# Optimization experiments

Measured on AMD Instinct MI355X. Metric: run time of the kernel, lower is better.

Reference implementation:

```python
import jax, jax.numpy as jnp
import numpy as np

B, S = 8192, 2048
EPS = 1e-8
DISCOUNT_FACTOR = 0.99
AVERAGE_LAMBDA = 0.9


def setup_inputs() -> dict:
    key = jax.random.key(0)
    k1, k2 = jax.random.split(key)
    values = jax.random.normal(k1, (B, S + 1, 1), dtype=jnp.float32)
    rewards = jax.random.normal(k2, (B, S, 1), dtype=jnp.float32)
    dones = jnp.zeros((B, S, 1), dtype=jnp.float32)
    # parameters initialized as in the module: atanh of target values
    raw_gamma = jnp.arctanh(jnp.full((1,), DISCOUNT_FACTOR, dtype=jnp.float32))
    raw_lambd = jnp.arctanh(jnp.full((S,), AVERAGE_LAMBDA, dtype=jnp.float32))
    return {"values": values, "rewards": rewards, "dones": dones,
            "raw_gamma": raw_gamma, "raw_lambd": raw_lambd}


def reference(values, rewards, dones, raw_gamma, raw_lambd):
    # gamma = tanh(raw_gamma).clamp_min(1e-8); lambda likewise (per timestep)
    gamma = jnp.maximum(jnp.tanh(raw_gamma), EPS)      # [1]
    lam = jnp.maximum(jnp.tanh(raw_lambd), EPS)        # [S]
    # time-major for scan: [S, B, 1]
    v_next = jnp.swapaxes(values[:, 1:], 0, 1)
    r = jnp.swapaxes(rewards, 0, 1)
    d = jnp.swapaxes(dones, 0, 1)

    def step(G, xs):
        vt1, rt, dt, lt = xs
        # G_t = r_t + gamma*(1-d_t)*((1-lam_t)*V_{t+1} + lam_t*G_{t+1})
        G = rt + gamma * (1.0 - dt) * ((1.0 - lt) * vt1 + lt * G)
        return G, G

    G_last = values[:, -1]  # bootstrap: [B, 1]
    _, Gs = jax.lax.scan(step, G_last, (v_next, r, d, lam), reverse=True)
    return jnp.swapaxes(Gs, 0, 1)  # [B, S, 1]
```

## Files before the change

kernel.cpp:

```cpp
#include <hip/hip_runtime.h>
#include <math.h>

#define EPS_F 1e-8f

typedef float vfloat4 __attribute__((ext_vector_type(4)));
typedef float uafloat4 __attribute__((ext_vector_type(4), aligned(4)));

__global__ __launch_bounds__(256) void glam_scan_kernel(
    const float* __restrict__ values,
    const float* __restrict__ rewards,
    const float* __restrict__ dones,
    const float* __restrict__ raw_gamma,
    const float* __restrict__ raw_lambd,
    float* __restrict__ out,
    int B)
{
    constexpr int S  = 2048;
    constexpr int NP = 8;

    __shared__ float lam_lds[S];

    const int tid  = threadIdx.x;
    const int wave = (blockIdx.x * blockDim.x + tid) >> 6;
    const int lane = tid & 63;

    #pragma unroll
    for (int k = 0; k < S / 256; ++k) {
        const int t = (k << 8) + tid;
        lam_lds[t] = fmaxf(tanhf(raw_lambd[t]), EPS_F);
    }
    __syncthreads();

    if (wave >= B) return;

    const float gamma = fmaxf(tanhf(raw_gamma[0]), EPS_F);

    const size_t vbase = (size_t)wave * (size_t)(S + 1);
    const size_t base  = (size_t)wave * (size_t)S;
    const int lo4 = 4 * lane;

    const float vS = values[vbase + S];

    float oA[NP][4], oP[NP][4];
    float pA[NP], pP[NP];

    #pragma unroll
    for (int p = 0; p < NP; ++p) {
        const int e0 = (p << 8) + lo4;

        const vfloat4 r4 = *reinterpret_cast<const vfloat4*>(rewards + base + e0);
        const vfloat4 d4 = *reinterpret_cast<const vfloat4*>(dones   + base + e0);

        const vfloat4 l4 = *reinterpret_cast<const vfloat4*>(&lam_lds[e0]);
        const float lamv[4] = { l4.x, l4.y, l4.z, l4.w };

        const uafloat4 v4 = *reinterpret_cast<const uafloat4*>(values + vbase + e0 + 1);
        const float v1[4] = { v4.x, v4.y, v4.z, v4.w };

        const float rr[4] = { r4.x, r4.y, r4.z, r4.w };
        const float dd[4] = { d4.x, d4.y, d4.z, d4.w };

        float a[4], bb[4];
        #pragma unroll
        for (int j = 0; j < 4; ++j) {
            const float c = gamma * (1.0f - dd[j]);
            a[j]  = fmaf(c * (1.0f - lamv[j]), v1[j], rr[j]);
            bb[j] = c * lamv[j];
        }

        float A = 0.0f, P = 1.0f;
        #pragma unroll
        for (int j = 3; j >= 0; --j) {
            A = fmaf(bb[j], A, a[j]);
            P *= bb[j];
        }

        #pragma unroll
        for (int d = 1; d < 64; d <<= 1) {
            float A2 = __shfl_down(A, d);
            float P2 = __shfl_down(P, d);
            const bool valid = (lane + d) < 64;
            A2 = valid ? A2 : 0.0f;
            P2 = valid ? P2 : 1.0f;
            A = fmaf(P, A2, A);
            P *= P2;
        }

        pA[p] = __shfl(A, 0);
        pP[p] = __shfl(P, 0);

        const float A1 = __shfl_down(A, 1);
        const float P1 = __shfl_down(P, 1);
        float Af = (lane == 63) ? 0.0f : A1;
        float Pf = (lane == 63) ? 1.0f : P1;

        #pragma unroll
        for (int j = 3; j >= 0; --j) {
            Af = fmaf(bb[j], Af, a[j]);
            Pf = bb[j] * Pf;
            oA[p][j] = Af;
            oP[p][j] = Pf;
        }
    }

    float Gb = vS;
    #pragma unroll
    for (int p = NP - 1; p >= 0; --p) {
        vfloat4 o4;
        o4.x = fmaf(oP[p][0], Gb, oA[p][0]);
        o4.y = fmaf(oP[p][1], Gb, oA[p][1]);
        o4.z = fmaf(oP[p][2], Gb, oA[p][2]);
        o4.w = fmaf(oP[p][3], Gb, oA[p][3]);
        __builtin_nontemporal_store(o4,
            reinterpret_cast<vfloat4*>(out + base + (p << 8) + lo4));
        Gb = fmaf(pP[p], Gb, pA[p]);
    }
}

__global__ void glam_naive_kernel(const float* __restrict__ values,
                                  const float* __restrict__ rewards,
                                  const float* __restrict__ dones,
                                  const float* __restrict__ raw_gamma,
                                  const float* __restrict__ raw_lambd,
                                  float* __restrict__ out, int B, int S) {
    int b = blockIdx.x * blockDim.x + threadIdx.x;
    if (b >= B) return;
    const float gamma = fmaxf(tanhf(raw_gamma[0]), EPS_F);
    const size_t vbase = (size_t)b * (size_t)(S + 1);
    const size_t base  = (size_t)b * (size_t)S;
    float G = values[vbase + S];
    for (int t = S - 1; t >= 0; --t) {
        const float lt = fmaxf(tanhf(raw_lambd[t]), EPS_F);
        const float c  = gamma * (1.0f - dones[base + t]);
        G = rewards[base + t] + c * ((1.0f - lt) * values[vbase + t + 1] + lt * G);
        out[base + t] = G;
    }
}

extern "C" void kernel_launch(void* const* d_in, const int* in_sizes, int n_in,
                              void* d_out, int out_size, void* d_ws, size_t ws_size,
                              hipStream_t stream) {
    const float* values    = (const float*)d_in[0];
    const float* rewards   = (const float*)d_in[1];
    const float* dones     = (const float*)d_in[2];
    const float* raw_gamma = (const float*)d_in[3];
    const float* raw_lambd = (const float*)d_in[4];
    float* out = (float*)d_out;

    const int S = in_sizes[4];
    const int B = in_sizes[1] / S;

    if (S != 2048) {
        glam_naive_kernel<<<(B + 255) / 256, 256, 0, stream>>>(
            values, rewards, dones, raw_gamma, raw_lambd, out, B, S);
        return;
    }

    const int total_threads = B * 64;
    const int blocks = (total_threads + 255) / 256;

    glam_scan_kernel<<<blocks, 256, 0, stream>>>(
        values, rewards, dones, raw_gamma, raw_lambd, out, B);
}
```

Before: 47.43 us.

## Batch all loads up front, split scan phases, use readfirstlane broadcast

Restructures the per-wave scan into phases. All global loads for the 8 chunks are issued first so memory latency overlaps, then the wave-level scans run for every chunk. The chunk carries are combined serially, and each output is finally recomputed by a short serial pass that starts from the resolved carry. The lane-0 broadcast now uses readfirstlane instead of a shuffle, and the stored oA/oP arrays are replaced by keeping a/bb live, which shifts register pressure.

```diff
diff --git a/kernel.cpp b/kernel.cpp
--- a/kernel.cpp
+++ b/kernel.cpp
@@ -5,6 +5,10 @@
 
 typedef float vfloat4 __attribute__((ext_vector_type(4)));
 typedef float uafloat4 __attribute__((ext_vector_type(4), aligned(4)));
+
+__device__ __forceinline__ float bcast0(float x) {
+    return __uint_as_float(__builtin_amdgcn_readfirstlane(__float_as_uint(x)));
+}
 
 __global__ __launch_bounds__(256) void glam_scan_kernel(
     const float* __restrict__ values,
@@ -41,40 +45,39 @@
 
     const float vS = values[vbase + S];
 
-    float oA[NP][4], oP[NP][4];
-    float pA[NP], pP[NP];
-
+    float a[NP][4], bb[NP][4];
     #pragma unroll
     for (int p = 0; p < NP; ++p) {
         const int e0 = (p << 8) + lo4;
 
-        const vfloat4 r4 = *reinterpret_cast<const vfloat4*>(rewards + base + e0);
-        const vfloat4 d4 = *reinterpret_cast<const vfloat4*>(dones   + base + e0);
-
-        const vfloat4 l4 = *reinterpret_cast<const vfloat4*>(&lam_lds[e0]);
-        const float lamv[4] = { l4.x, l4.y, l4.z, l4.w };
-
+        const vfloat4  r4 = *reinterpret_cast<const vfloat4*>(rewards + base + e0);
+        const vfloat4  d4 = *reinterpret_cast<const vfloat4*>(dones   + base + e0);
         const uafloat4 v4 = *reinterpret_cast<const uafloat4*>(values + vbase + e0 + 1);
-        const float v1[4] = { v4.x, v4.y, v4.z, v4.w };
+        const vfloat4  l4 = *reinterpret_cast<const vfloat4*>(&lam_lds[e0]);
 
         const float rr[4] = { r4.x, r4.y, r4.z, r4.w };
         const float dd[4] = { d4.x, d4.y, d4.z, d4.w };
+        const float vv[4] = { v4.x, v4.y, v4.z, v4.w };
+        const float ll[4] = { l4.x, l4.y, l4.z, l4.w };
 
-        float a[4], bb[4];
         #pragma unroll
         for (int j = 0; j < 4; ++j) {
             const float c = gamma * (1.0f - dd[j]);
-            a[j]  = fmaf(c * (1.0f - lamv[j]), v1[j], rr[j]);
-            bb[j] = c * lamv[j];
+            a[p][j]  = fmaf(c * (1.0f - ll[j]), vv[j], rr[j]);
+            bb[p][j] = c * ll[j];
         }
+    }
 
+    float A1[NP], P1[NP];
+    float pA[NP], pP[NP];
+    #pragma unroll
+    for (int p = 0; p < NP; ++p) {
         float A = 0.0f, P = 1.0f;
         #pragma unroll
         for (int j = 3; j >= 0; --j) {
-            A = fmaf(bb[j], A, a[j]);
-            P *= bb[j];
+            A = fmaf(bb[p][j], A, a[p][j]);
+            P *= bb[p][j];
         }
-
         #pragma unroll
         for (int d = 1; d < 64; d <<= 1) {
             float A2 = __shfl_down(A, d);
@@ -85,35 +88,33 @@
             A = fmaf(P, A2, A);
             P *= P2;
         }
+        pA[p] = bcast0(A);
+        pP[p] = bcast0(P);
+        const float Ad = __shfl_down(A, 1);
+        const float Pd = __shfl_down(P, 1);
+        A1[p] = (lane == 63) ? 0.0f : Ad;
+        P1[p] = (lane == 63) ? 1.0f : Pd;
+    }
 
-        pA[p] = __shfl(A, 0);
-        pP[p] = __shfl(P, 0);
+    float Gb[NP + 1];
+    Gb[NP] = vS;
+    #pragma unroll
+    for (int p = NP - 1; p >= 0; --p)
+        Gb[p] = fmaf(pP[p], Gb[p + 1], pA[p]);
 
-        const float A1 = __shfl_down(A, 1);
-        const float P1 = __shfl_down(P, 1);
-        float Af = (lane == 63) ? 0.0f : A1;
-        float Pf = (lane == 63) ? 1.0f : P1;
-
+    #pragma unroll
+    for (int p = 0; p < NP; ++p) {
+        float G = fmaf(P1[p], Gb[p + 1], A1[p]);
+        float o[4];
         #pragma unroll
         for (int j = 3; j >= 0; --j) {
-            Af = fmaf(bb[j], Af, a[j]);
-            Pf = bb[j] * Pf;
-            oA[p][j] = Af;
-            oP[p][j] = Pf;
+            G = fmaf(bb[p][j], G, a[p][j]);
+            o[j] = G;
         }
-    }
-
-    float Gb = vS;
-    #pragma unroll
-    for (int p = NP - 1; p >= 0; --p) {
         vfloat4 o4;
-        o4.x = fmaf(oP[p][0], Gb, oA[p][0]);
-        o4.y = fmaf(oP[p][1], Gb, oA[p][1]);
-        o4.z = fmaf(oP[p][2], Gb, oA[p][2]);
-        o4.w = fmaf(oP[p][3], Gb, oA[p][3]);
+        o4.x = o[0]; o4.y = o[1]; o4.z = o[2]; o4.w = o[3];
         __builtin_nontemporal_store(o4,
             reinterpret_cast<vfloat4*>(out + base + (p << 8) + lo4));
-        Gb = fmaf(pP[p], Gb, pA[p]);
     }
 }
 
```

New measurement: 48.72 us. +2.7%, slower.
